# Performance work log

Measured on AMD Instinct MI355X. Metric: run time of the kernel, lower is better.

The kernel has to match this reference:

```python
import jax, jax.numpy as jnp
import numpy as np

EMBED = 1024
HEADS = 16
HEAD_DIM = EMBED // HEADS


def setup_inputs() -> dict:
    key = jax.random.key(0)
    ks = jax.random.split(key, 11)
    B, S, D = 2, 2048, EMBED
    scale = 1.0 / np.sqrt(D)
    inp = {
        "q": jax.random.normal(ks[0], (B, S, D), jnp.float32),
        "k": jax.random.normal(ks[1], (B, S, D), jnp.float32),
        "v": jax.random.normal(ks[2], (B, S, D), jnp.float32),
        "Wq": jax.random.normal(ks[3], (D, D), jnp.float32) * scale,
        "bq": jnp.zeros((D,), jnp.float32),
        "Wk": jax.random.normal(ks[4], (D, D), jnp.float32) * scale,
        "bk": jnp.zeros((D,), jnp.float32),
        "Wv": jax.random.normal(ks[5], (D, D), jnp.float32) * scale,
        "bv": jnp.zeros((D,), jnp.float32),
        "Wo": jax.random.normal(ks[6], (D, D), jnp.float32) * scale,
        "bo": jnp.zeros((D,), jnp.float32),
    }
    return inp


def _split_heads(x):
    b, n, c = x.shape
    return x.reshape(b, n, HEADS, c // HEADS).transpose(0, 2, 1, 3)  # [b,h,n,dh]


def reference(q, k, v, Wq, bq, Wk, bk, Wv, bv, Wo, bo):
    qh = _split_heads(q @ Wq + bq)
    kh = _split_heads(k @ Wk + bk)
    vh = _split_heads(v @ Wv + bv)
    scale = 1.0 / jnp.sqrt(jnp.asarray(HEAD_DIM, qh.dtype))
    att = jnp.einsum("bhqd,bhkd->bhqk", qh, kh) * scale
    att = jax.nn.softmax(att, axis=-1)
    out = jnp.einsum("bhqk,bhkd->bhqd", att, vh)
    b, h, n, dh = out.shape
    out = out.transpose(0, 2, 1, 3).reshape(b, n, h * dh)
    return out @ Wo + bo
```

## Files before the change

### kernel.cpp

```cpp
#include <hip/hip_runtime.h>
#include <hip/hip_bf16.h>
#include <stdint.h>

typedef unsigned short u16;
typedef __bf16 bf16x8 __attribute__((ext_vector_type(8)));
typedef float f32x4 __attribute__((ext_vector_type(4)));
typedef unsigned int u32x4 __attribute__((ext_vector_type(4)));
typedef unsigned int u32x2 __attribute__((ext_vector_type(2)));

#define S_LEN 2048
#define DMODEL 1024
#define NHEAD 16
#define DHEAD 64
#define MROWS 4096

__device__ __forceinline__ u16 f2b(float f) {
  __hip_bfloat16 h = __float2bfloat16(f);
  union { __hip_bfloat16 h; u16 u; } c;
  c.h = h;
  return c.u;
}
__device__ __forceinline__ unsigned int pk2(float lo, float hi) {
  return (unsigned int)f2b(lo) | ((unsigned int)f2b(hi) << 16);
}

__device__ __forceinline__ void gload16(const void* g, void* l) {
  __builtin_amdgcn_global_load_lds(
      (const __attribute__((address_space(1))) unsigned int*)(uintptr_t)g,
      (__attribute__((address_space(3))) unsigned int*)(uintptr_t)l,
      16, 0, 0);
}

__global__ __launch_bounds__(256) void prep(
    const float* __restrict__ q, const float* __restrict__ k, const float* __restrict__ v,
    const float* __restrict__ Wq, const float* __restrict__ Wk,
    const float* __restrict__ Wv, const float* __restrict__ Wo,
    u16* __restrict__ Qx, u16* __restrict__ Kx, u16* __restrict__ Vx,
    u16* __restrict__ Wqt, u16* __restrict__ Wkt,
    u16* __restrict__ Wvt, u16* __restrict__ Wot) {
  __shared__ u16 tile[64][65];
  const int z = blockIdx.z;
  const int tid = threadIdx.x;
  if (z < 3) {
    const float* src = (z == 0) ? q : (z == 1) ? k : v;
    u16* dst = (z == 0) ? Qx : (z == 1) ? Kx : Vx;
    const size_t i8 = ((size_t)blockIdx.x * 256 + tid) * 8;
    float4 a = *(const float4*)(src + i8);
    float4 b = *(const float4*)(src + i8 + 4);
    u16 o[8];
    o[0] = f2b(a.x); o[1] = f2b(a.y); o[2] = f2b(a.z); o[3] = f2b(a.w);
    o[4] = f2b(b.x); o[5] = f2b(b.y); o[6] = f2b(b.z); o[7] = f2b(b.w);
    *(u32x4*)(dst + i8) = *(const u32x4*)o;
    return;
  }
  if (blockIdx.x >= 256) return;
  const int zz = z - 3;
  const float* W = (zz == 0) ? Wq : (zz == 1) ? Wk : (zz == 2) ? Wv : Wo;
  u16* Wt = (zz == 0) ? Wqt : (zz == 1) ? Wkt : (zz == 2) ? Wvt : Wot;
  const int n0 = (blockIdx.x & 15) * 64, k0 = (blockIdx.x >> 4) * 64;
#pragma unroll
  for (int j = 0; j < 16; j++) {
    int idx = j * 256 + tid;
    int r = idx >> 6, c = idx & 63;
    tile[r][c] = f2b(W[(size_t)(k0 + r) * DMODEL + n0 + c]);
  }
  __syncthreads();
#pragma unroll
  for (int j = 0; j < 16; j++) {
    int idx = j * 256 + tid;
    int r = idx >> 6, c = idx & 63;
    Wt[(size_t)(n0 + r) * DMODEL + k0 + c] = tile[c][r];
  }
}

template <int MODE>
__device__ __forceinline__ void gemm_body(const u16* __restrict__ A,
                                          const u16* __restrict__ Bt,
                                          const float* __restrict__ bias,
                                          void* __restrict__ Cv) {
  constexpr int K = DMODEL;
  __shared__ u16 As[128 * 32];
  __shared__ u16 Bs[128 * 32];
  const int tid = threadIdx.x;
  const int wave = tid >> 6, lane = tid & 63;
  const int quad = lane >> 4, l15 = lane & 15;
  const int wr = wave >> 1, wc = wave & 1;
  const int lid = blockIdx.y * 8 + blockIdx.x;
  const int sw = (lid & 7) * 32 + (lid >> 3);
  const int bcol = sw & 7, brow = sw >> 3;

  f32x4 acc[4][4] = {};

  for (int k0 = 0; k0 < K; k0 += 32) {
    __syncthreads();
#pragma unroll
    for (int t = 0; t < 2; t++) {
      const int slot = t * 256 + wave * 64 + lane;
      const int row = slot >> 2;
      const int col = (slot & 3) << 3;
      const int ldsb = (t * 256 + wave * 64) * 8;
      gload16(A + (size_t)(brow * 128 + row) * K + k0 + col, As + ldsb);
      gload16(Bt + (size_t)(bcol * 128 + row) * K + k0 + col, Bs + ldsb);
    }
    __syncthreads();

    bf16x8 af[4], bfm[4];
#pragma unroll
    for (int i = 0; i < 4; i++)
      af[i] = *(const bf16x8*)(As + (wr * 64 + i * 16 + l15) * 32 + quad * 8);
#pragma unroll
    for (int j = 0; j < 4; j++)
      bfm[j] = *(const bf16x8*)(Bs + (wc * 64 + j * 16 + l15) * 32 + quad * 8);
#pragma unroll
    for (int i = 0; i < 4; i++)
#pragma unroll
      for (int j = 0; j < 4; j++)
        acc[i][j] = __builtin_amdgcn_mfma_f32_16x16x32_bf16(af[i], bfm[j], acc[i][j], 0, 0, 0);
  }

#pragma unroll
  for (int i = 0; i < 4; i++)
#pragma unroll
    for (int j = 0; j < 4; j++) {
      const int col = bcol * 128 + wc * 64 + j * 16 + l15;
      const float bv = bias[col];
      if (MODE == 2) {
        const int srow = brow * 128 + wr * 64 + i * 16 + quad * 4;
        const int bb = srow >> 11, s = srow & (S_LEN - 1);
        u32x2 pd;
        pd.x = pk2(acc[i][j][0] + bv, acc[i][j][1] + bv);
        pd.y = pk2(acc[i][j][2] + bv, acc[i][j][3] + bv);
        *(u32x2*)((u16*)Cv + ((size_t)(bb * 1024 + col)) * S_LEN + s) = pd;
      } else {
#pragma unroll
        for (int r = 0; r < 4; r++) {
          const int row = brow * 128 + wr * 64 + i * 16 + quad * 4 + r;
          if (MODE == 1)
            ((float*)Cv)[(size_t)row * DMODEL + col] = acc[i][j][r] + bv;
          else
            ((u16*)Cv)[(size_t)row * DMODEL + col] = f2b(acc[i][j][r] + bv);
        }
      }
    }
}

__global__ __launch_bounds__(256) void gemm_qkv(
    const u16* __restrict__ Qx, const u16* __restrict__ Kx, const u16* __restrict__ Vx,
    const u16* __restrict__ Wqt, const u16* __restrict__ Wkt, const u16* __restrict__ Wvt,
    const float* __restrict__ bq, const float* __restrict__ bk, const float* __restrict__ bv,
    u16* __restrict__ Qp, u16* __restrict__ Kp, u16* __restrict__ Vt) {
  const int z = blockIdx.z;
  if (z == 2) {
    gemm_body<2>(Vx, Wvt, bv, Vt);
  } else {
    const u16* A = (z == 0) ? Qx : Kx;
    const u16* Bt = (z == 0) ? Wqt : Wkt;
    const float* bias = (z == 0) ? bq : bk;
    u16* C = (z == 0) ? Qp : Kp;
    gemm_body<0>(A, Bt, bias, C);
  }
}

__global__ __launch_bounds__(256) void gemm_out(
    const u16* __restrict__ A, const u16* __restrict__ Bt,
    const float* __restrict__ bias, float* __restrict__ C) {
  gemm_body<1>(A, Bt, bias, C);
}

#define EXP2SCALE 0.180336880112f

#define ISSUE_KV(ksb, vsb)              \
  do {                                  \
    gload16(pK0, (ksb) + dstu);         \
    gload16(pK1, (ksb) + 2048 + dstu);  \
    gload16(pV0, (vsb) + dstu);         \
    gload16(pV1, (vsb) + 2048 + dstu);  \
    pK0 += 64 * DMODEL; pK1 += 64 * DMODEL; \
    pV0 += 64; pV1 += 64;               \
  } while (0)

#define TILE_COMPUTE(ksb, vsb)                                                   \
  do {                                                                           \
    f32x4 sfT[4] = {};                                                           \
    __builtin_amdgcn_s_setprio(1);                                               \
    _Pragma("unroll") for (int n = 0; n < 4; n++) {                              \
      _Pragma("unroll") for (int kx = 0; kx < 2; kx++) {                         \
        bf16x8 ka = *(const bf16x8*)((ksb) +                                     \
            ((((n * 16 + l15) * 64) + kx * 32 + quad * 8) ^ ((l15 & 7) << 3)));  \
        sfT[n] = __builtin_amdgcn_mfma_f32_16x16x32_bf16(ka, qf[kx], sfT[n], 0, 0, 0); \
      }                                                                          \
    }                                                                            \
    __builtin_amdgcn_s_setprio(0);                                               \
    _Pragma("unroll") for (int n = 0; n < 4; n++) {                              \
      float p0 = __builtin_amdgcn_exp2f(sfT[n][0] * EXP2SCALE);                  \
      float p1 = __builtin_amdgcn_exp2f(sfT[n][1] * EXP2SCALE);                  \
      float p2 = __builtin_amdgcn_exp2f(sfT[n][2] * EXP2SCALE);                  \
      float p3 = __builtin_amdgcn_exp2f(sfT[n][3] * EXP2SCALE);                  \
      u32x2 pd;                                                                  \
      pd.x = pk2(p0, p1);                                                        \
      pd.y = pk2(p2, p3);                                                        \
      int prow = wave * 16 + l15;                                                \
      *(u32x2*)(Ps + ((prow * 64 + n * 16 + quad * 4) ^ ((prow & 7) << 3))) = pd;\
    }                                                                            \
    __builtin_amdgcn_s_setprio(1);                                               \
    _Pragma("unroll") for (int kx = 0; kx < 2; kx++) {                           \
      int prow = wave * 16 + l15;                                                \
      bf16x8 ap = *(const bf16x8*)(Ps +                                          \
          ((prow * 64 + kx * 32 + quad * 8) ^ ((prow & 7) << 3)));               \
      lacc = __builtin_amdgcn_mfma_f32_16x16x32_bf16(ap, b1, lacc, 0, 0, 0);     \
      _Pragma("unroll") for (int n = 0; n < 4; n++) {                            \
        bf16x8 bv = *(const bf16x8*)((vsb) +                                     \
            ((((n * 16 + l15) * 64) + kx * 32 + quad * 8) ^ ((l15 & 7) << 3)));  \
        oacc[n] = __builtin_amdgcn_mfma_f32_16x16x32_bf16(ap, bv, oacc[n], 0, 0, 0); \
      }                                                                          \
    }                                                                            \
    __builtin_amdgcn_s_setprio(0);                                               \
  } while (0)

__global__ __launch_bounds__(256) void attn(const u16* __restrict__ Qp,
                                            const u16* __restrict__ Kp,
                                            const u16* __restrict__ Vt,
                                            u16* __restrict__ Op) {
  __shared__ u16 Ks0[64 * 64], Ks1[64 * 64];
  __shared__ u16 Vs0[64 * 64], Vs1[64 * 64];
  __shared__ u16 Ps[64 * 64];

  const int tid = threadIdx.x;
  const int wave = tid >> 6, lane = tid & 63;
  const int quad = lane >> 4, l15 = lane & 15;
  const int b = blockIdx.z, h = blockIdx.y, s0 = blockIdx.x * 64;

  const size_t baseK = ((size_t)(b * S_LEN)) * DMODEL + h * DHEAD;
  const size_t baseV = ((size_t)((b * NHEAD + h) * DHEAD)) * S_LEN;

  const int r0 = tid >> 3;
  const int cg = (tid & 7) ^ (r0 & 7);
  const u16* pK0 = Kp + baseK + (size_t)r0 * DMODEL + cg * 8;
  const u16* pK1 = pK0 + (size_t)32 * DMODEL;
  const u16* pV0 = Vt + baseV + (size_t)r0 * S_LEN + cg * 8;
  const u16* pV1 = pV0 + (size_t)32 * S_LEN;
  const int dstu = wave * 512;

  bf16x8 b1;
  {
    union { u16 a[8]; bf16x8 v; } c;
    u16 one = (l15 == 0) ? 0x3F80 : 0;
#pragma unroll
    for (int j = 0; j < 8; j++) c.a[j] = one;
    b1 = c.v;
  }

  bf16x8 qf[2];
#pragma unroll
  for (int kx = 0; kx < 2; kx++)
    qf[kx] = *(const bf16x8*)(Qp +
        ((size_t)(b * S_LEN + s0 + wave * 16 + l15)) * DMODEL +
        h * DHEAD + kx * 32 + quad * 8);

  f32x4 oacc[4] = {};
  f32x4 lacc = {};

  ISSUE_KV(Ks0, Vs0);

#pragma unroll 1
  for (int kt = 0; kt < 32; kt += 2) {
    __syncthreads();
    ISSUE_KV(Ks1, Vs1);
    TILE_COMPUTE(Ks0, Vs0);
    __syncthreads();
    if (kt + 2 < 32) ISSUE_KV(Ks0, Vs0);
    TILE_COMPUTE(Ks1, Vs1);
  }

  float inv[4];
#pragma unroll
  for (int r = 0; r < 4; r++)
    inv[r] = 1.0f / __shfl(lacc[r], quad * 16);
#pragma unroll
  for (int n = 0; n < 4; n++)
#pragma unroll
    for (int r = 0; r < 4; r++) {
      int row = s0 + wave * 16 + quad * 4 + r;
      int col = h * DHEAD + n * 16 + l15;
      Op[((size_t)(b * S_LEN + row)) * DMODEL + col] = f2b(oacc[n][r] * inv[r]);
    }
}

extern "C" void kernel_launch(void* const* d_in, const int* in_sizes, int n_in,
                              void* d_out, int out_size, void* d_ws, size_t ws_size,
                              hipStream_t stream) {
  const float* q  = (const float*)d_in[0];
  const float* k  = (const float*)d_in[1];
  const float* v  = (const float*)d_in[2];
  const float* Wq = (const float*)d_in[3];
  const float* bq = (const float*)d_in[4];
  const float* Wk = (const float*)d_in[5];
  const float* bk = (const float*)d_in[6];
  const float* Wv = (const float*)d_in[7];
  const float* bv = (const float*)d_in[8];
  const float* Wo = (const float*)d_in[9];
  const float* bo = (const float*)d_in[10];

  char* w = (char*)d_ws;
  const size_t WSZ = (size_t)DMODEL * DMODEL * 2;
  const size_t XSZ = (size_t)MROWS * DMODEL * 2;
  u16* Wqt = (u16*)(w);
  u16* Wkt = (u16*)(w + WSZ);
  u16* Wvt = (u16*)(w + 2 * WSZ);
  u16* Wot = (u16*)(w + 3 * WSZ);
  u16* Qx  = (u16*)(w + 4 * WSZ);
  u16* Kx  = (u16*)(w + 4 * WSZ + XSZ);
  u16* Vx  = (u16*)(w + 4 * WSZ + 2 * XSZ);
  u16* Qp  = (u16*)(w + 4 * WSZ + 3 * XSZ);
  u16* Kp  = (u16*)(w + 4 * WSZ + 4 * XSZ);
  u16* Vt  = (u16*)(w + 4 * WSZ + 5 * XSZ);
  u16* Op  = (u16*)(w + 4 * WSZ + 6 * XSZ);

  prep<<<dim3(2048, 1, 7), 256, 0, stream>>>(q, k, v, Wq, Wk, Wv, Wo,
                                             Qx, Kx, Vx, Wqt, Wkt, Wvt, Wot);
  gemm_qkv<<<dim3(8, 32, 3), 256, 0, stream>>>(Qx, Kx, Vx, Wqt, Wkt, Wvt,
                                               bq, bk, bv, Qp, Kp, Vt);
  attn<<<dim3(32, 16, 2), 256, 0, stream>>>(Qp, Kp, Vt, Op);
  gemm_out<<<dim3(8, 32, 1), 256, 0, stream>>>(Op, Wot, bo, (float*)d_out);
}
```

Before: 233.1 us.

## Switch attention to 32x32 MFMA with in-register P and larger query tiles

Rewrites the attention inner loop to use 32x32x16 bf16 MFMAs. The exp'd scores stay in registers, rearranged with permlane32 swaps and packed with v_cvt_pk_bf16_f32, so the LDS round-trip for P is gone. Each block now covers 128 query rows, with 32 per wave, which halves the grid and the K/V reloads, and block IDs are swizzled across heads and batches. The exp2 scale is folded into the Q projection epilogue. The cost is higher register pressure, and the softmax still has no max subtraction, as before.

```diff
diff --git a/kernel.cpp b/kernel.cpp
--- a/kernel.cpp
+++ b/kernel.cpp
@@ -5,6 +5,7 @@
 typedef unsigned short u16;
 typedef __bf16 bf16x8 __attribute__((ext_vector_type(8)));
 typedef float f32x4 __attribute__((ext_vector_type(4)));
+typedef float f32x16 __attribute__((ext_vector_type(16)));
 typedef unsigned int u32x4 __attribute__((ext_vector_type(4)));
 typedef unsigned int u32x2 __attribute__((ext_vector_type(2)));
 
@@ -13,6 +14,7 @@
 #define NHEAD 16
 #define DHEAD 64
 #define MROWS 4096
+#define EXP2SCALE 0.180336880112f
 
 __device__ __forceinline__ u16 f2b(float f) {
   __hip_bfloat16 h = __float2bfloat16(f);
@@ -22,6 +24,16 @@
 }
 __device__ __forceinline__ unsigned int pk2(float lo, float hi) {
   return (unsigned int)f2b(lo) | ((unsigned int)f2b(hi) << 16);
+}
+__device__ __forceinline__ unsigned int cvtpk(float a, float b) {
+  unsigned int r;
+  asm("v_cvt_pk_bf16_f32 %0, %1, %2" : "=v"(r) : "v"(a), "v"(b));
+  return r;
+}
+__device__ __forceinline__ void plswap(unsigned int &a, unsigned int &b) {
+  auto r = __builtin_amdgcn_permlane32_swap((int)a, (int)b, false, false);
+  a = (unsigned int)r[0];
+  b = (unsigned int)r[1];
 }
 
 __device__ __forceinline__ void gload16(const void* g, void* l) {
@@ -137,6 +149,8 @@
           const int row = brow * 128 + wr * 64 + i * 16 + quad * 4 + r;
           if (MODE == 1)
             ((float*)Cv)[(size_t)row * DMODEL + col] = acc[i][j][r] + bv;
+          else if (MODE == 3)
+            ((u16*)Cv)[(size_t)row * DMODEL + col] = f2b((acc[i][j][r] + bv) * EXP2SCALE);
           else
             ((u16*)Cv)[(size_t)row * DMODEL + col] = f2b(acc[i][j][r] + bv);
         }
@@ -152,12 +166,10 @@
   const int z = blockIdx.z;
   if (z == 2) {
     gemm_body<2>(Vx, Wvt, bv, Vt);
+  } else if (z == 0) {
+    gemm_body<3>(Qx, Wqt, bq, Qp);
   } else {
-    const u16* A = (z == 0) ? Qx : Kx;
-    const u16* Bt = (z == 0) ? Wqt : Wkt;
-    const float* bias = (z == 0) ? bq : bk;
-    u16* C = (z == 0) ? Qp : Kp;
-    gemm_body<0>(A, Bt, bias, C);
+    gemm_body<0>(Kx, Wkt, bk, Kp);
   }
 }
 
@@ -166,8 +178,6 @@
     const float* __restrict__ bias, float* __restrict__ C) {
   gemm_body<1>(A, Bt, bias, C);
 }
-
-#define EXP2SCALE 0.180336880112f
 
 #define ISSUE_KV(ksb, vsb)              \
   do {                                  \
@@ -179,42 +189,42 @@
     pV0 += 64; pV1 += 64;               \
   } while (0)
 
-#define TILE_COMPUTE(ksb, vsb)                                                   \
-  do {                                                                           \
-    f32x4 sfT[4] = {};                                                           \
-    __builtin_amdgcn_s_setprio(1);                                               \
-    _Pragma("unroll") for (int n = 0; n < 4; n++) {                              \
-      _Pragma("unroll") for (int kx = 0; kx < 2; kx++) {                         \
-        bf16x8 ka = *(const bf16x8*)((ksb) +                                     \
-            ((((n * 16 + l15) * 64) + kx * 32 + quad * 8) ^ ((l15 & 7) << 3)));  \
-        sfT[n] = __builtin_amdgcn_mfma_f32_16x16x32_bf16(ka, qf[kx], sfT[n], 0, 0, 0); \
-      }                                                                          \
-    }                                                                            \
-    __builtin_amdgcn_s_setprio(0);                                               \
-    _Pragma("unroll") for (int n = 0; n < 4; n++) {                              \
-      float p0 = __builtin_amdgcn_exp2f(sfT[n][0] * EXP2SCALE);                  \
-      float p1 = __builtin_amdgcn_exp2f(sfT[n][1] * EXP2SCALE);                  \
-      float p2 = __builtin_amdgcn_exp2f(sfT[n][2] * EXP2SCALE);                  \
-      float p3 = __builtin_amdgcn_exp2f(sfT[n][3] * EXP2SCALE);                  \
-      u32x2 pd;                                                                  \
-      pd.x = pk2(p0, p1);                                                        \
-      pd.y = pk2(p2, p3);                                                        \
-      int prow = wave * 16 + l15;                                                \
-      *(u32x2*)(Ps + ((prow * 64 + n * 16 + quad * 4) ^ ((prow & 7) << 3))) = pd;\
-    }                                                                            \
-    __builtin_amdgcn_s_setprio(1);                                               \
-    _Pragma("unroll") for (int kx = 0; kx < 2; kx++) {                           \
-      int prow = wave * 16 + l15;                                                \
-      bf16x8 ap = *(const bf16x8*)(Ps +                                          \
-          ((prow * 64 + kx * 32 + quad * 8) ^ ((prow & 7) << 3)));               \
-      lacc = __builtin_amdgcn_mfma_f32_16x16x32_bf16(ap, b1, lacc, 0, 0, 0);     \
-      _Pragma("unroll") for (int n = 0; n < 4; n++) {                            \
-        bf16x8 bv = *(const bf16x8*)((vsb) +                                     \
-            ((((n * 16 + l15) * 64) + kx * 32 + quad * 8) ^ ((l15 & 7) << 3)));  \
-        oacc[n] = __builtin_amdgcn_mfma_f32_16x16x32_bf16(ap, bv, oacc[n], 0, 0, 0); \
-      }                                                                          \
-    }                                                                            \
-    __builtin_amdgcn_s_setprio(0);                                               \
+#define TILE_COMPUTE(ksb, vsb)                                                     \
+  do {                                                                             \
+    f32x16 sA = {}, sB = {};                                                       \
+    __builtin_amdgcn_s_setprio(1);                                                 \
+    _Pragma("unroll") for (int c = 0; c < 4; c++) {                                \
+      bf16x8 ka0 = *(const bf16x8*)((ksb) + off[c]);                               \
+      bf16x8 ka1 = *(const bf16x8*)((ksb) + off[c] + 2048);                        \
+      sA = __builtin_amdgcn_mfma_f32_32x32x16_bf16(ka0, qf[c], sA, 0, 0, 0);       \
+      sB = __builtin_amdgcn_mfma_f32_32x32x16_bf16(ka1, qf[c], sB, 0, 0, 0);       \
+    }                                                                              \
+    __builtin_amdgcn_s_setprio(0);                                                 \
+    bf16x8 pf[4];                                                                  \
+    _Pragma("unroll") for (int kb = 0; kb < 2; kb++) {                             \
+      const f32x16 s = kb ? sB : sA;                                               \
+      unsigned int cc[8];                                                          \
+      _Pragma("unroll") for (int m = 0; m < 8; m++)                                \
+        cc[m] = cvtpk(__builtin_amdgcn_exp2f(s[2 * m]),                            \
+                      __builtin_amdgcn_exp2f(s[2 * m + 1]));                       \
+      plswap(cc[0], cc[2]);                                                        \
+      plswap(cc[1], cc[3]);                                                        \
+      plswap(cc[4], cc[6]);                                                        \
+      plswap(cc[5], cc[7]);                                                        \
+      union { unsigned int u[4]; bf16x8 v; } f0, f1;                               \
+      f0.u[0] = cc[0]; f0.u[1] = cc[1]; f0.u[2] = cc[2]; f0.u[3] = cc[3];          \
+      f1.u[0] = cc[4]; f1.u[1] = cc[5]; f1.u[2] = cc[6]; f1.u[3] = cc[7];          \
+      pf[2 * kb] = f0.v; pf[2 * kb + 1] = f1.v;                                    \
+    }                                                                              \
+    __builtin_amdgcn_s_setprio(1);                                                 \
+    _Pragma("unroll") for (int g = 0; g < 4; g++) {                                \
+      bf16x8 v0 = *(const bf16x8*)((vsb) + off[g]);                                \
+      bf16x8 v1 = *(const bf16x8*)((vsb) + off[g] + 2048);                         \
+      lacc  = __builtin_amdgcn_mfma_f32_32x32x16_bf16(pf[g], ones, lacc, 0, 0, 0); \
+      oacc0 = __builtin_amdgcn_mfma_f32_32x32x16_bf16(pf[g], v0, oacc0, 0, 0, 0);  \
+      oacc1 = __builtin_amdgcn_mfma_f32_32x32x16_bf16(pf[g], v1, oacc1, 0, 0, 0);  \
+    }                                                                              \
+    __builtin_amdgcn_s_setprio(0);                                                 \
   } while (0)
 
 __global__ __launch_bounds__(256) void attn(const u16* __restrict__ Qp,
@@ -223,12 +233,15 @@
                                             u16* __restrict__ Op) {
   __shared__ u16 Ks0[64 * 64], Ks1[64 * 64];
   __shared__ u16 Vs0[64 * 64], Vs1[64 * 64];
-  __shared__ u16 Ps[64 * 64];
 
   const int tid = threadIdx.x;
   const int wave = tid >> 6, lane = tid & 63;
-  const int quad = lane >> 4, l15 = lane & 15;
-  const int b = blockIdx.z, h = blockIdx.y, s0 = blockIdx.x * 64;
+  const int row31 = lane & 31, hl = lane >> 5;
+
+  const int id = blockIdx.x + (blockIdx.y << 4) + (blockIdx.z << 8);
+  const int sw = ((id & 7) << 6) + (id >> 3);
+  const int qt = sw & 15, h = (sw >> 4) & 15, b = sw >> 8;
+  const int s0 = qt * 128;
 
   const size_t baseK = ((size_t)(b * S_LEN)) * DMODEL + h * DHEAD;
   const size_t baseV = ((size_t)((b * NHEAD + h) * DHEAD)) * S_LEN;
@@ -241,24 +254,28 @@
   const u16* pV1 = pV0 + (size_t)32 * S_LEN;
   const int dstu = wave * 512;
 
-  bf16x8 b1;
+  int off[4];
+#pragma unroll
+  for (int c = 0; c < 4; c++)
+    off[c] = row31 * 64 + ((((c << 1) + hl) ^ (row31 & 7)) << 3);
+
+  bf16x8 ones;
   {
     union { u16 a[8]; bf16x8 v; } c;
-    u16 one = (l15 == 0) ? 0x3F80 : 0;
-#pragma unroll
-    for (int j = 0; j < 8; j++) c.a[j] = one;
-    b1 = c.v;
-  }
-
-  bf16x8 qf[2];
-#pragma unroll
-  for (int kx = 0; kx < 2; kx++)
-    qf[kx] = *(const bf16x8*)(Qp +
-        ((size_t)(b * S_LEN + s0 + wave * 16 + l15)) * DMODEL +
-        h * DHEAD + kx * 32 + quad * 8);
-
-  f32x4 oacc[4] = {};
-  f32x4 lacc = {};
+#pragma unroll
+    for (int j = 0; j < 8; j++) c.a[j] = 0x3F80;
+    ones = c.v;
+  }
+
+  bf16x8 qf[4];
+#pragma unroll
+  for (int c = 0; c < 4; c++)
+    qf[c] = *(const bf16x8*)(Qp +
+        ((size_t)(b * S_LEN + s0 + wave * 32 + row31)) * DMODEL +
+        h * DHEAD + c * 16 + hl * 8);
+
+  f32x16 oacc0 = {}, oacc1 = {};
+  f32x16 lacc = {};
 
   ISSUE_KV(Ks0, Vs0);
 
@@ -272,18 +289,14 @@
     TILE_COMPUTE(Ks1, Vs1);
   }
 
-  float inv[4];
-#pragma unroll
-  for (int r = 0; r < 4; r++)
-    inv[r] = 1.0f / __shfl(lacc[r], quad * 16);
-#pragma unroll
-  for (int n = 0; n < 4; n++)
-#pragma unroll
-    for (int r = 0; r < 4; r++) {
-      int row = s0 + wave * 16 + quad * 4 + r;
-      int col = h * DHEAD + n * 16 + l15;
-      Op[((size_t)(b * S_LEN + row)) * DMODEL + col] = f2b(oacc[n][r] * inv[r]);
-    }
+#pragma unroll
+  for (int r = 0; r < 16; r++) {
+    const float inv = 1.0f / lacc[r];
+    const int qrow = (r & 3) + 8 * (r >> 2) + 4 * hl;
+    const size_t rb = ((size_t)(b * S_LEN + s0 + wave * 32 + qrow)) * DMODEL + h * DHEAD;
+    Op[rb + row31]      = f2b(oacc0[r] * inv);
+    Op[rb + 32 + row31] = f2b(oacc1[r] * inv);
+  }
 }
 
 extern "C" void kernel_launch(void* const* d_in, const int* in_sizes, int n_in,
@@ -320,6 +333,6 @@
                                              Qx, Kx, Vx, Wqt, Wkt, Wvt, Wot);
   gemm_qkv<<<dim3(8, 32, 3), 256, 0, stream>>>(Qx, Kx, Vx, Wqt, Wkt, Wvt,
                                                bq, bk, bv, Qp, Kp, Vt);
-  attn<<<dim3(32, 16, 2), 256, 0, stream>>>(Qp, Kp, Vt, Op);
+  attn<<<dim3(16, 16, 2), 256, 0, stream>>>(Qp, Kp, Vt, Op);
   gemm_out<<<dim3(8, 32, 1), 256, 0, stream>>>(Op, Wot, bo, (float*)d_out);
 }
```

After: 221.7 us. 1.05x faster.
